# Optimization experiments

Measured on AMD Instinct MI355X. Metric: run time of the kernel, lower is better.

## Reference

```python
import jax, jax.numpy as jnp
import numpy as np

B, L, D, P, H = 2, 512, 512, 64, 2048
BASE_FREQ = 10000.0


def _make_pos_freq(L, P, base=BASE_FREQ):
    # RoPE-style per-position frequencies: pos_freq[l, p] = l * base**(-p/P)
    inv_freq = base ** (-jnp.arange(P, dtype=jnp.float32) / P)
    pos = jnp.arange(L, dtype=jnp.float32)
    return pos[:, None] * inv_freq[None, :]  # (L, P)


def setup_inputs() -> dict:
    key = jax.random.key(0)
    ks = jax.random.split(key, 7)
    s = 0.02
    return {
        "x_real": jax.random.normal(ks[0], (B, L, D), dtype=jnp.float32),
        "x_imag": jax.random.normal(ks[1], (B, L, P), dtype=jnp.float32),
        "pos_freq": _make_pos_freq(L, P),
        "W_up": jax.random.normal(ks[2], (D, H), dtype=jnp.float32) * s,
        "w": jax.random.normal(ks[3], (P, H), dtype=jnp.float32) * s,
        "b": jax.random.normal(ks[4], (P, H), dtype=jnp.float32) * s,
        "W_down_real": jax.random.normal(ks[5], (H, D), dtype=jnp.float32) * s,
        "W_down_imag": jax.random.normal(ks[6], (H, P), dtype=jnp.float32) * s,
    }


def reference(x_real, x_imag, pos_freq, W_up, w, b, W_down_real, W_down_imag):
    energy_scale = 1.0 / np.sqrt(w.shape[0])
    # Omniware gate: theta = w * (x_imag * pos_freq) + b, summed cosines over P
    time_content = x_imag * pos_freq[None]                 # (B, L, P)
    theta = time_content[..., None] * w + b                # (B, L, P, H)
    gate = jnp.cos(theta).sum(axis=-2) * energy_scale      # (B, L, H)
    # Value path (no activation, GLU-style)
    value = jnp.einsum('bld,dh->blh', x_real, W_up)        # (B, L, H)
    out = value * gate                                     # (B, L, H)
    # Separate down projections + additive residuals
    out_real = x_real + jnp.einsum('blh,hd->bld', out, W_down_real)
    out_imag = x_imag + jnp.einsum('blh,hp->blp', gate, W_down_imag)
    return out_real, out_imag
```

## Files before the change

### kernel.cpp

```cpp
#include <hip/hip_runtime.h>

#define DEV __device__ __forceinline__

typedef __attribute__((ext_vector_type(4))) float  f32x4;
typedef __attribute__((ext_vector_type(8))) short  short8v;
typedef __attribute__((ext_vector_type(4))) short  short4v;

static constexpr int Bq = 2, Lq = 512, Dq = 512, Pq = 64, Hq = 2048;
static constexpr int BLq = Bq * Lq;
static constexpr float INV2PI = 0.15915494309189535f;

DEV short f2bf(float f) {
  unsigned u = __float_as_uint(f);
  u += 0x7fffu + ((u >> 16) & 1u);
  return (short)(u >> 16);
}
DEV float bf2f(short s) {
  return __uint_as_float(((unsigned)(unsigned short)s) << 16);
}

DEV float cos_rev(float t) {
#if __has_builtin(__builtin_amdgcn_fractf) && __has_builtin(__builtin_amdgcn_cosf)
  return __builtin_amdgcn_cosf(__builtin_amdgcn_fractf(t));
#else
  return __cosf((t - floorf(t)) * 6.283185307179586f);
#endif
}

DEV void gload_lds16(const void* g, void* l) {
  __builtin_amdgcn_global_load_lds(
      (const __attribute__((address_space(1))) void*)g,
      (__attribute__((address_space(3))) void*)l, 16, 0, 0);
}

__global__ __launch_bounds__(256) void fused_prologue(
    const float* __restrict__ x_real, const float* __restrict__ x_imag,
    const float* __restrict__ pos_freq,
    const float* __restrict__ W_up, const float* __restrict__ wq,
    const float* __restrict__ bq, const float* __restrict__ Wdr,
    const float* __restrict__ Wdi,
    short* __restrict__ wupT, short* __restrict__ wdrT,
    short* __restrict__ wdiT, short* __restrict__ xrbf,
    short* __restrict__ gate) {
  __shared__ __align__(16) float smem[32 * 33];
  const int b = blockIdx.x, tid = threadIdx.x;

  if (b < 2176) {
    const float* in; short* out; int R, C, c0, r0;
    if (b < 1024)      { in = W_up; out = wupT; R = 512;  C = 2048; c0 = (b & 63) * 32; r0 = (b >> 6) * 32; }
    else if (b < 2048) { int bb = b - 1024; in = Wdr; out = wdrT; R = 2048; C = 512; c0 = (bb & 15) * 32; r0 = (bb >> 4) * 32; }
    else               { int bb = b - 2048; in = Wdi; out = wdiT; R = 2048; C = 64;  c0 = (bb & 1) * 32;  r0 = (bb >> 1) * 32; }
    float (*tile)[33] = (float(*)[33])smem;
    const int tx = tid & 31, ty = tid >> 5;
#pragma unroll
    for (int i = 0; i < 4; ++i)
      tile[ty + 8 * i][tx] = in[(r0 + ty + 8 * i) * C + c0 + tx];
    __syncthreads();
#pragma unroll
    for (int i = 0; i < 4; ++i)
      out[(c0 + ty + 8 * i) * R + r0 + tx] = f2bf(tile[tx][ty + 8 * i]);

  } else if (b < 2688) {
    const int i = ((b - 2176) * 256 + tid) * 4;
    f32x4 v = *(const f32x4*)&x_real[i];
    short4v s;
    s.x = f2bf(v.x); s.y = f2bf(v.y); s.z = f2bf(v.z); s.w = f2bf(v.w);
    *(short4v*)&xrbf[i] = s;

  } else {
    constexpr int BLT = 16;
    float (*tc)[64] = (float(*)[64])smem;
    const int g = b - 2688;
    const int bl0 = (g & 63) * BLT;
    const int h = (g >> 6) * 256 + tid;

#pragma unroll
    for (int e = 0; e < BLT * 64 / 256; ++e) {
      int f = tid + 256 * e;
      int r = f >> 6, p = f & 63;
      int bl = bl0 + r;
      int l = bl & (Lq - 1);
      tc[r][p] = x_imag[bl * Pq + p] * pos_freq[l * Pq + p];
    }
    __syncthreads();

    float acc[BLT] = {};
#pragma unroll 1
    for (int p = 0; p < Pq; p += 4) {
      float wv0 = wq[(p + 0) * Hq + h] * INV2PI, wv1 = wq[(p + 1) * Hq + h] * INV2PI;
      float wv2 = wq[(p + 2) * Hq + h] * INV2PI, wv3 = wq[(p + 3) * Hq + h] * INV2PI;
      float bv0 = bq[(p + 0) * Hq + h] * INV2PI, bv1 = bq[(p + 1) * Hq + h] * INV2PI;
      float bv2 = bq[(p + 2) * Hq + h] * INV2PI, bv3 = bq[(p + 3) * Hq + h] * INV2PI;
#pragma unroll
      for (int r = 0; r < BLT; ++r) {
        f32x4 t = *(const f32x4*)&tc[r][p];
        acc[r] += cos_rev(t.x * wv0 + bv0);
        acc[r] += cos_rev(t.y * wv1 + bv1);
        acc[r] += cos_rev(t.z * wv2 + bv2);
        acc[r] += cos_rev(t.w * wv3 + bv3);
      }
    }
#pragma unroll
    for (int r = 0; r < BLT; ++r)
      gate[(bl0 + r) * Hq + h] = f2bf(acc[r] * 0.125f);
  }
}

template <int NSTEPS>
DEV void mfma_core(const short* __restrict__ Arow, int lda,
                   const short* __restrict__ Brow, int ldb,
                   short* As0, short* Bs0, short* As1, short* Bs1,
                   int tid, f32x4* acc) {
  const int lane = tid & 63;
  const int wv = tid >> 6, wr = wv >> 1, wc = wv & 1;
  const int lrow = lane & 15, lk = (lane >> 4) * 8;
  const int srow = tid >> 2, sseg = (tid & 3) * 8;

  auto stage = [&](short* As, short* Bs, int k0) {
    if (tid < 128)
      gload_lds16(&Arow[srow * lda + k0 + sseg], &As[tid * 8]);
    gload_lds16(&Brow[srow * ldb + k0 + sseg], &Bs[tid * 8]);
  };
  auto compute = [&](const short* As, const short* Bs) {
    short8v a  = *(const short8v*)&As[(wr * 16 + lrow) * 32 + lk];
    short8v b0 = *(const short8v*)&Bs[(wc * 32 + lrow) * 32 + lk];
    short8v b1 = *(const short8v*)&Bs[(wc * 32 + 16 + lrow) * 32 + lk];
    acc[0] = __builtin_amdgcn_mfma_f32_16x16x32_bf16(a, b0, acc[0], 0, 0, 0);
    acc[1] = __builtin_amdgcn_mfma_f32_16x16x32_bf16(a, b1, acc[1], 0, 0, 0);
  };

  stage(As0, Bs0, 0);
  __syncthreads();
#pragma unroll 1
  for (int t = 0; t < NSTEPS; t += 2) {
    if (t + 1 < NSTEPS) stage(As1, Bs1, (t + 1) * 32);
    compute(As0, Bs0);
    __syncthreads();
    if (t + 2 < NSTEPS) stage(As0, Bs0, (t + 2) * 32);
    if (t + 1 < NSTEPS) compute(As1, Bs1);
    __syncthreads();
  }
}

__global__ __launch_bounds__(256) void fused_up(
    const short* __restrict__ xrbf, const short* __restrict__ wupT,
    const short* __restrict__ gate, short* __restrict__ outbf) {
  __shared__ __align__(16) short As[2][32 * 32];
  __shared__ __align__(16) short Bs[2][64 * 32];
  const int tid = threadIdx.x;
  const int m0 = (blockIdx.x >> 5) * 32, n0 = (blockIdx.x & 31) * 64;
  const int lane = tid & 63, wv = tid >> 6, wr = wv >> 1, wc = wv & 1;
  const int lrow = lane & 15;

  f32x4 acc[2] = {};
  mfma_core<16>(&xrbf[m0 * Dq], Dq, &wupT[n0 * Dq], Dq,
                As[0], Bs[0], As[1], Bs[1], tid, acc);

#pragma unroll
  for (int j = 0; j < 2; ++j)
#pragma unroll
    for (int r = 0; r < 4; ++r) {
      int row = m0 + wr * 16 + (lane >> 4) * 4 + r;
      int col = n0 + wc * 32 + j * 16 + lrow;
      outbf[row * Hq + col] = f2bf(acc[j][r] * bf2f(gate[row * Hq + col]));
    }
}

__global__ __launch_bounds__(256) void fused_down(
    const short* __restrict__ outbf, const short* __restrict__ wdrT,
    const short* __restrict__ gate, const short* __restrict__ wdiT,
    const float* __restrict__ x_real, const float* __restrict__ x_imag,
    float* __restrict__ out_real, float* __restrict__ out_imag) {
  __shared__ __align__(16) short As[2][32 * 32];
  __shared__ __align__(16) short Bs[2][64 * 32];
  const int b = blockIdx.x, tid = threadIdx.x;
  const int lane = tid & 63, wv = tid >> 6, wr = wv >> 1, wc = wv & 1;
  const int lrow = lane & 15;
  f32x4 acc[2] = {};

  if (b < 256) {
    const int m0 = (b >> 3) * 32, n0 = (b & 7) * 64;
    mfma_core<64>(&outbf[m0 * Hq], Hq, &wdrT[n0 * Hq], Hq,
                  As[0], Bs[0], As[1], Bs[1], tid, acc);
#pragma unroll
    for (int j = 0; j < 2; ++j)
#pragma unroll
      for (int r = 0; r < 4; ++r) {
        int row = m0 + wr * 16 + (lane >> 4) * 4 + r;
        int col = n0 + wc * 32 + j * 16 + lrow;
        out_real[row * Dq + col] = x_real[row * Dq + col] + acc[j][r];
      }
  } else {
    const int m0 = (b - 256) * 32;
    mfma_core<64>(&gate[m0 * Hq], Hq, wdiT, Hq,
                  As[0], Bs[0], As[1], Bs[1], tid, acc);
#pragma unroll
    for (int j = 0; j < 2; ++j)
#pragma unroll
      for (int r = 0; r < 4; ++r) {
        int row = m0 + wr * 16 + (lane >> 4) * 4 + r;
        int col = wc * 32 + j * 16 + lrow;
        out_imag[row * Pq + col] = x_imag[row * Pq + col] + acc[j][r];
      }
  }
}

extern "C" void kernel_launch(void* const* d_in, const int* in_sizes, int n_in,
                              void* d_out, int out_size, void* d_ws,
                              size_t ws_size, hipStream_t stream) {
  const float* x_real   = (const float*)d_in[0];
  const float* x_imag   = (const float*)d_in[1];
  const float* pos_freq = (const float*)d_in[2];
  const float* W_up     = (const float*)d_in[3];
  const float* wq       = (const float*)d_in[4];
  const float* bq       = (const float*)d_in[5];
  const float* Wdr      = (const float*)d_in[6];
  const float* Wdi      = (const float*)d_in[7];

  float* out_real = (float*)d_out;
  float* out_imag = out_real + BLq * Dq;

  char* ws = (char*)d_ws;
  short* gate_bf = (short*)ws;
  short* outbf   = (short*)(ws + (4u << 20));
  short* wupT    = (short*)(ws + (8u << 20));
  short* wdrT    = (short*)(ws + (10u << 20));
  short* xrbf    = (short*)(ws + (12u << 20));
  short* wdiT    = (short*)(ws + (13u << 20));

  fused_prologue<<<3200, 256, 0, stream>>>(
      x_real, x_imag, pos_freq, W_up, wq, bq, Wdr, Wdi,
      wupT, wdrT, wdiT, xrbf, gate_bf);

  fused_up<<<1024, 256, 0, stream>>>(xrbf, wupT, gate_bf, outbf);

  fused_down<<<288, 256, 0, stream>>>(
      outbf, wdrT, gate_bf, wdiT, x_real, x_imag, out_real, out_imag);
}
```

Baseline: 129.2 us.

## Reorder prologue blocks, halve gate tile, prefetch weights, single-buffer GEMM staging

The prologue now puts the cosine-gate blocks first and shrinks each block's row tile from 16 to 8, which doubles the gate block count so those blocks spread across more CUs and start earlier. The gate loop loads the next group of w/b coefficients while computing the current one, hiding global load latency. The MFMA core drops LDS double buffering in favour of one buffer with two barriers per k-step, which simplifies the code and cuts LDS use but exposes load latency inside the GEMMs. The grid grows to 3712 blocks to cover the new gate tiling.

```diff
diff --git a/kernel.cpp b/kernel.cpp
--- a/kernel.cpp
+++ b/kernel.cpp
@@ -45,34 +45,11 @@
   __shared__ __align__(16) float smem[32 * 33];
   const int b = blockIdx.x, tid = threadIdx.x;
 
-  if (b < 2176) {
-    const float* in; short* out; int R, C, c0, r0;
-    if (b < 1024)      { in = W_up; out = wupT; R = 512;  C = 2048; c0 = (b & 63) * 32; r0 = (b >> 6) * 32; }
-    else if (b < 2048) { int bb = b - 1024; in = Wdr; out = wdrT; R = 2048; C = 512; c0 = (bb & 15) * 32; r0 = (bb >> 4) * 32; }
-    else               { int bb = b - 2048; in = Wdi; out = wdiT; R = 2048; C = 64;  c0 = (bb & 1) * 32;  r0 = (bb >> 1) * 32; }
-    float (*tile)[33] = (float(*)[33])smem;
-    const int tx = tid & 31, ty = tid >> 5;
-#pragma unroll
-    for (int i = 0; i < 4; ++i)
-      tile[ty + 8 * i][tx] = in[(r0 + ty + 8 * i) * C + c0 + tx];
-    __syncthreads();
-#pragma unroll
-    for (int i = 0; i < 4; ++i)
-      out[(c0 + ty + 8 * i) * R + r0 + tx] = f2bf(tile[tx][ty + 8 * i]);
-
-  } else if (b < 2688) {
-    const int i = ((b - 2176) * 256 + tid) * 4;
-    f32x4 v = *(const f32x4*)&x_real[i];
-    short4v s;
-    s.x = f2bf(v.x); s.y = f2bf(v.y); s.z = f2bf(v.z); s.w = f2bf(v.w);
-    *(short4v*)&xrbf[i] = s;
-
-  } else {
-    constexpr int BLT = 16;
+  if (b < 1024) {
+    constexpr int BLT = 8;
     float (*tc)[64] = (float(*)[64])smem;
-    const int g = b - 2688;
-    const int bl0 = (g & 63) * BLT;
-    const int h = (g >> 6) * 256 + tid;
+    const int bl0 = (b & 127) * BLT;
+    const int h = (b >> 7) * 256 + tid;
 
 #pragma unroll
     for (int e = 0; e < BLT * 64 / 256; ++e) {
@@ -84,60 +61,88 @@
     }
     __syncthreads();
 
+    const float* wp = wq + h;
+    const float* bp = bq + h;
     float acc[BLT] = {};
+    float cw0 = wp[0 * Hq] * INV2PI, cw1 = wp[1 * Hq] * INV2PI;
+    float cw2 = wp[2 * Hq] * INV2PI, cw3 = wp[3 * Hq] * INV2PI;
+    float cb0 = bp[0 * Hq] * INV2PI, cb1 = bp[1 * Hq] * INV2PI;
+    float cb2 = bp[2 * Hq] * INV2PI, cb3 = bp[3 * Hq] * INV2PI;
 #pragma unroll 1
     for (int p = 0; p < Pq; p += 4) {
-      float wv0 = wq[(p + 0) * Hq + h] * INV2PI, wv1 = wq[(p + 1) * Hq + h] * INV2PI;
-      float wv2 = wq[(p + 2) * Hq + h] * INV2PI, wv3 = wq[(p + 3) * Hq + h] * INV2PI;
-      float bv0 = bq[(p + 0) * Hq + h] * INV2PI, bv1 = bq[(p + 1) * Hq + h] * INV2PI;
-      float bv2 = bq[(p + 2) * Hq + h] * INV2PI, bv3 = bq[(p + 3) * Hq + h] * INV2PI;
+      float nw0, nw1, nw2, nw3, nb0, nb1, nb2, nb3;
+      if (p + 4 < Pq) {
+        nw0 = wp[(p + 4) * Hq]; nw1 = wp[(p + 5) * Hq];
+        nw2 = wp[(p + 6) * Hq]; nw3 = wp[(p + 7) * Hq];
+        nb0 = bp[(p + 4) * Hq]; nb1 = bp[(p + 5) * Hq];
+        nb2 = bp[(p + 6) * Hq]; nb3 = bp[(p + 7) * Hq];
+      } else {
+        nw0 = nw1 = nw2 = nw3 = nb0 = nb1 = nb2 = nb3 = 0.f;
+      }
 #pragma unroll
       for (int r = 0; r < BLT; ++r) {
         f32x4 t = *(const f32x4*)&tc[r][p];
-        acc[r] += cos_rev(t.x * wv0 + bv0);
-        acc[r] += cos_rev(t.y * wv1 + bv1);
-        acc[r] += cos_rev(t.z * wv2 + bv2);
-        acc[r] += cos_rev(t.w * wv3 + bv3);
-      }
+        acc[r] += cos_rev(t.x * cw0 + cb0);
+        acc[r] += cos_rev(t.y * cw1 + cb1);
+        acc[r] += cos_rev(t.z * cw2 + cb2);
+        acc[r] += cos_rev(t.w * cw3 + cb3);
+      }
+      cw0 = nw0 * INV2PI; cw1 = nw1 * INV2PI;
+      cw2 = nw2 * INV2PI; cw3 = nw3 * INV2PI;
+      cb0 = nb0 * INV2PI; cb1 = nb1 * INV2PI;
+      cb2 = nb2 * INV2PI; cb3 = nb3 * INV2PI;
     }
 #pragma unroll
     for (int r = 0; r < BLT; ++r)
       gate[(bl0 + r) * Hq + h] = f2bf(acc[r] * 0.125f);
+
+  } else if (b < 3200) {
+    const int bb = b - 1024;
+    const float* in; short* out; int R, C, c0, r0;
+    if (bb < 1024)      { in = W_up; out = wupT; R = 512;  C = 2048; c0 = (bb & 63) * 32; r0 = (bb >> 6) * 32; }
+    else if (bb < 2048) { int t2 = bb - 1024; in = Wdr; out = wdrT; R = 2048; C = 512; c0 = (t2 & 15) * 32; r0 = (t2 >> 4) * 32; }
+    else                { int t2 = bb - 2048; in = Wdi; out = wdiT; R = 2048; C = 64;  c0 = (t2 & 1) * 32;  r0 = (t2 >> 1) * 32; }
+    float (*tile)[33] = (float(*)[33])smem;
+    const int tx = tid & 31, ty = tid >> 5;
+#pragma unroll
+    for (int i = 0; i < 4; ++i)
+      tile[ty + 8 * i][tx] = in[(r0 + ty + 8 * i) * C + c0 + tx];
+    __syncthreads();
+#pragma unroll
+    for (int i = 0; i < 4; ++i)
+      out[(c0 + ty + 8 * i) * R + r0 + tx] = f2bf(tile[tx][ty + 8 * i]);
+
+  } else {
+    const int i = ((b - 3200) * 256 + tid) * 4;
+    f32x4 v = *(const f32x4*)&x_real[i];
+    short4v s;
+    s.x = f2bf(v.x); s.y = f2bf(v.y); s.z = f2bf(v.z); s.w = f2bf(v.w);
+    *(short4v*)&xrbf[i] = s;
   }
 }
 
 template <int NSTEPS>
 DEV void mfma_core(const short* __restrict__ Arow, int lda,
                    const short* __restrict__ Brow, int ldb,
-                   short* As0, short* Bs0, short* As1, short* Bs1,
-                   int tid, f32x4* acc) {
+                   short* As, short* Bs, int tid, f32x4* acc) {
   const int lane = tid & 63;
   const int wv = tid >> 6, wr = wv >> 1, wc = wv & 1;
   const int lrow = lane & 15, lk = (lane >> 4) * 8;
   const int srow = tid >> 2, sseg = (tid & 3) * 8;
 
-  auto stage = [&](short* As, short* Bs, int k0) {
+#pragma unroll 1
+  for (int t = 0; t < NSTEPS; ++t) {
+    const int k0 = t * 32;
     if (tid < 128)
       gload_lds16(&Arow[srow * lda + k0 + sseg], &As[tid * 8]);
     gload_lds16(&Brow[srow * ldb + k0 + sseg], &Bs[tid * 8]);
-  };
-  auto compute = [&](const short* As, const short* Bs) {
+    __syncthreads();
+
     short8v a  = *(const short8v*)&As[(wr * 16 + lrow) * 32 + lk];
     short8v b0 = *(const short8v*)&Bs[(wc * 32 + lrow) * 32 + lk];
     short8v b1 = *(const short8v*)&Bs[(wc * 32 + 16 + lrow) * 32 + lk];
     acc[0] = __builtin_amdgcn_mfma_f32_16x16x32_bf16(a, b0, acc[0], 0, 0, 0);
     acc[1] = __builtin_amdgcn_mfma_f32_16x16x32_bf16(a, b1, acc[1], 0, 0, 0);
-  };
-
-  stage(As0, Bs0, 0);
-  __syncthreads();
-#pragma unroll 1
-  for (int t = 0; t < NSTEPS; t += 2) {
-    if (t + 1 < NSTEPS) stage(As1, Bs1, (t + 1) * 32);
-    compute(As0, Bs0);
-    __syncthreads();
-    if (t + 2 < NSTEPS) stage(As0, Bs0, (t + 2) * 32);
-    if (t + 1 < NSTEPS) compute(As1, Bs1);
     __syncthreads();
   }
 }
@@ -145,16 +150,15 @@
 __global__ __launch_bounds__(256) void fused_up(
     const short* __restrict__ xrbf, const short* __restrict__ wupT,
     const short* __restrict__ gate, short* __restrict__ outbf) {
-  __shared__ __align__(16) short As[2][32 * 32];
-  __shared__ __align__(16) short Bs[2][64 * 32];
+  __shared__ __align__(16) short As[32 * 32];
+  __shared__ __align__(16) short Bs[64 * 32];
   const int tid = threadIdx.x;
   const int m0 = (blockIdx.x >> 5) * 32, n0 = (blockIdx.x & 31) * 64;
   const int lane = tid & 63, wv = tid >> 6, wr = wv >> 1, wc = wv & 1;
   const int lrow = lane & 15;
 
   f32x4 acc[2] = {};
-  mfma_core<16>(&xrbf[m0 * Dq], Dq, &wupT[n0 * Dq], Dq,
-                As[0], Bs[0], As[1], Bs[1], tid, acc);
+  mfma_core<16>(&xrbf[m0 * Dq], Dq, &wupT[n0 * Dq], Dq, As, Bs, tid, acc);
 
 #pragma unroll
   for (int j = 0; j < 2; ++j)
@@ -171,8 +175,8 @@
     const short* __restrict__ gate, const short* __restrict__ wdiT,
     const float* __restrict__ x_real, const float* __restrict__ x_imag,
     float* __restrict__ out_real, float* __restrict__ out_imag) {
-  __shared__ __align__(16) short As[2][32 * 32];
-  __shared__ __align__(16) short Bs[2][64 * 32];
+  __shared__ __align__(16) short As[32 * 32];
+  __shared__ __align__(16) short Bs[64 * 32];
   const int b = blockIdx.x, tid = threadIdx.x;
   const int lane = tid & 63, wv = tid >> 6, wr = wv >> 1, wc = wv & 1;
   const int lrow = lane & 15;
@@ -180,8 +184,7 @@
 
   if (b < 256) {
     const int m0 = (b >> 3) * 32, n0 = (b & 7) * 64;
-    mfma_core<64>(&outbf[m0 * Hq], Hq, &wdrT[n0 * Hq], Hq,
-                  As[0], Bs[0], As[1], Bs[1], tid, acc);
+    mfma_core<64>(&outbf[m0 * Hq], Hq, &wdrT[n0 * Hq], Hq, As, Bs, tid, acc);
 #pragma unroll
     for (int j = 0; j < 2; ++j)
 #pragma unroll
@@ -192,8 +195,7 @@
       }
   } else {
     const int m0 = (b - 256) * 32;
-    mfma_core<64>(&gate[m0 * Hq], Hq, wdiT, Hq,
-                  As[0], Bs[0], As[1], Bs[1], tid, acc);
+    mfma_core<64>(&gate[m0 * Hq], Hq, wdiT, Hq, As, Bs, tid, acc);
 #pragma unroll
     for (int j = 0; j < 2; ++j)
 #pragma unroll
@@ -228,7 +230,7 @@
   short* xrbf    = (short*)(ws + (12u << 20));
   short* wdiT    = (short*)(ws + (13u << 20));
 
-  fused_prologue<<<3200, 256, 0, stream>>>(
+  fused_prologue<<<3712, 256, 0, stream>>>(
       x_real, x_imag, pos_freq, W_up, wq, bq, Wdr, Wdi,
       wupT, wdrT, wdiT, xrbf, gate_bf);
 
```

Result: slower. 136.2 us (+5.5%).
